# Optimization experiments

Measured on AMD Instinct MI355X. Metric: run time of the kernel, lower is better.

Reference implementation:

```python
import jax, jax.numpy as jnp
import numpy as np

N_NODES = 100000
N_EDGES = 3200000
F_IN = 128
F_OUT = 128


def setup_inputs() -> dict:
    key = jax.random.key(0)
    k1, k2, k3 = jax.random.split(key, 3)
    x = jax.random.normal(k1, (N_NODES, F_IN), dtype=jnp.float32)
    edge_index = jax.random.randint(k2, (2, N_EDGES), 0, N_NODES, dtype=jnp.int64)
    # xavier_uniform for weight, zeros for bias
    limit = float(np.sqrt(6.0 / (F_IN + F_OUT)))
    weight = jax.random.uniform(k3, (F_IN, F_OUT), dtype=jnp.float32,
                                minval=-limit, maxval=limit)
    bias = jnp.zeros((F_OUT,), dtype=jnp.float32)
    return {"x": x, "edge_index": edge_index, "weight": weight, "bias": bias}


def reference(x, edge_index, weight, bias):
    num_nodes = x.shape[0]
    # add self loops
    loops = jnp.arange(num_nodes, dtype=edge_index.dtype)
    row = jnp.concatenate([edge_index[0], loops])  # [E+N]
    col = jnp.concatenate([edge_index[1], loops])  # [E+N]
    # degree from row (matches torch.bincount(row))
    deg = jnp.zeros((num_nodes,), dtype=x.dtype).at[row].add(1.0)
    deg_inv_sqrt = jnp.where(deg > 0, jax.lax.rsqrt(jnp.maximum(deg, 1.0)), 0.0)
    norm = deg_inv_sqrt[row] * deg_inv_sqrt[col]  # [E+N]
    # dense transform then sparse aggregation (gather-scale-scatter)
    support = x @ weight  # [N, F_OUT]
    msgs = support[col] * norm[:, None]  # [E+N, F_OUT]
    out = jax.ops.segment_sum(msgs, row, num_segments=num_nodes)
    return out + bias
```

## Files before the change

kernel.cpp:

```cpp
#include <hip/hip_runtime.h>
#include <hip/hip_fp16.h>

#define FDIM 128
#define SCAN_B 1024
#define NCHK 128
#define NHALF 2
#define NFB (NHALF * NCHK)

typedef _Float16 half8 __attribute__((ext_vector_type(8)));
typedef float f32x4 __attribute__((ext_vector_type(4)));

__global__ void __launch_bounds__(1024) k_cnt(const int* __restrict__ row,
                                              unsigned char* __restrict__ cnt8,
                                              int nE, int n, int hspan) {
    __shared__ unsigned int h32[12544];
    int half  = blockIdx.x & (NHALF - 1);
    int chunk = blockIdx.x >> 1;
    int lo  = half * hspan;
    int len = min(hspan, n - lo);
    int nw  = (len + 3) >> 2;
    for (int j = threadIdx.x; j < nw; j += 1024) h32[j] = 0;
    __syncthreads();

    int per = (((nE + NCHK - 1) / NCHK) + 3) & ~3;
    int beg = chunk * per;
    int end = min(beg + per, nE);
    if (beg < end) {
        int nv = (end - beg) >> 2;
        const int4* row4 = reinterpret_cast<const int4*>(row + beg);
        for (int q = threadIdx.x; q < nv; q += 1024) {
            int4 r = row4[q];
            unsigned a;
            a = (unsigned)(r.x - lo); if (a < (unsigned)len) atomicAdd(&h32[a >> 2], 1u << ((a & 3) << 3));
            a = (unsigned)(r.y - lo); if (a < (unsigned)len) atomicAdd(&h32[a >> 2], 1u << ((a & 3) << 3));
            a = (unsigned)(r.z - lo); if (a < (unsigned)len) atomicAdd(&h32[a >> 2], 1u << ((a & 3) << 3));
            a = (unsigned)(r.w - lo); if (a < (unsigned)len) atomicAdd(&h32[a >> 2], 1u << ((a & 3) << 3));
        }
        for (int e = beg + (nv << 2) + threadIdx.x; e < end; e += 1024) {
            unsigned a = (unsigned)(row[e] - lo);
            if (a < (unsigned)len) atomicAdd(&h32[a >> 2], 1u << ((a & 3) << 3));
        }
    }
    __syncthreads();
    unsigned int* dst = reinterpret_cast<unsigned int*>(cnt8 + (size_t)chunk * n + lo);
    for (int j = threadIdx.x; j < nw; j += 1024) dst[j] = h32[j];
}

__global__ void __launch_bounds__(1024) k_scan_reduce(const unsigned char* __restrict__ cnt8,
                                                      int* __restrict__ part, int n) {
    __shared__ int sd[1024];
    int i = blockIdx.x * SCAN_B + threadIdx.x;
    int v = 0;
    if (i < n) {
        v = 1;
        const unsigned char* p = cnt8 + i;
        #pragma unroll 16
        for (int c = 0; c < NCHK; ++c) v += p[(size_t)c * n];
    }
    sd[threadIdx.x] = v;
    __syncthreads();
    for (int off = 512; off > 0; off >>= 1) {
        if (threadIdx.x < off) sd[threadIdx.x] += sd[threadIdx.x + off];
        __syncthreads();
    }
    if (threadIdx.x == 0) part[blockIdx.x] = sd[0];
}

__global__ void __launch_bounds__(1024) k_scan_final(unsigned char* __restrict__ cnt8,
                                                     const int* __restrict__ part,
                                                     int* __restrict__ offs,
                                                     float* __restrict__ dis,
                                                     int* __restrict__ sc,
                                                     int n, int nb) {
    __shared__ int sd[1024];
    __shared__ int sdp[128];
    int pv = 0;
    if (threadIdx.x < 128) {
        pv = (threadIdx.x < nb) ? part[threadIdx.x] : 0;
        sdp[threadIdx.x] = pv;
    }
    __syncthreads();
    for (int off = 1; off < 128; off <<= 1) {
        int t = 0;
        if (threadIdx.x < 128 && threadIdx.x >= off) t = sdp[threadIdx.x - off];
        __syncthreads();
        if (threadIdx.x < 128) sdp[threadIdx.x] += t;
        __syncthreads();
    }
    int blockbase = (blockIdx.x == 0) ? 0 : sdp[blockIdx.x - 1];

    int i = blockIdx.x * SCAN_B + threadIdx.x;
    int v = 0;
    if (i < n) {
        v = 1;
        const unsigned char* p = cnt8 + i;
        #pragma unroll 16
        for (int c = 0; c < NCHK; ++c) v += p[(size_t)c * n];
    }
    sd[threadIdx.x] = v;
    __syncthreads();
    for (int off = 1; off < 1024; off <<= 1) {
        int t = (threadIdx.x >= off) ? sd[threadIdx.x - off] : 0;
        __syncthreads();
        sd[threadIdx.x] += t;
        __syncthreads();
    }
    if (i < n) {
        int o = blockbase + sd[threadIdx.x] - v;
        offs[i] = o;
        if (i == n - 1) offs[n] = o + v;
        dis[i]  = rsqrtf((float)v);
        sc[o]   = i;
        unsigned char* p = cnt8 + i;
        int b = 1;
        #pragma unroll 16
        for (int c = 0; c < NCHK; ++c) {
            unsigned char cb = p[(size_t)c * n];
            p[(size_t)c * n] = (unsigned char)b;
            b += cb;
        }
    }
}

__global__ void __launch_bounds__(1024) k_fuse(const int* __restrict__ row,
                                               const int* __restrict__ col,
                                               unsigned char* __restrict__ cnt8,
                                               const int* __restrict__ offs,
                                               int* __restrict__ sc,
                                               const float* __restrict__ x,
                                               const float* __restrict__ w,
                                               const float* __restrict__ dis,
                                               __half* __restrict__ support,
                                               int nE, int n, int hspan) {
    __shared__ char smraw[65536];

    if (blockIdx.x < NFB) {
        unsigned int* cur32 = reinterpret_cast<unsigned int*>(smraw);
        int half  = blockIdx.x & (NHALF - 1);
        int chunk = blockIdx.x >> 1;
        int lo  = half * hspan;
        int len = min(hspan, n - lo);
        int nw  = (len + 3) >> 2;
        const unsigned int* src = reinterpret_cast<const unsigned int*>(
            cnt8 + (size_t)chunk * n + lo);
        for (int j = threadIdx.x; j < nw; j += 1024) cur32[j] = src[j];
        __syncthreads();

        int per = (((nE + NCHK - 1) / NCHK) + 3) & ~3;
        int beg = chunk * per;
        int end = min(beg + per, nE);
        if (beg < end) {
            int nv = (end - beg) >> 2;
            const int4* row4 = reinterpret_cast<const int4*>(row + beg);
            const int4* col4 = reinterpret_cast<const int4*>(col + beg);
            for (int q = threadIdx.x; q < nv; q += 1024) {
                int4 r  = row4[q];
                int4 cc = col4[q];
                unsigned a, old, sh;
                a = (unsigned)(r.x - lo);
                if (a < (unsigned)len) {
                    sh = (a & 3) << 3;
                    old = atomicAdd(&cur32[a >> 2], 1u << sh);
                    sc[offs[r.x] + (int)((old >> sh) & 255u)] = cc.x;
                }
                a = (unsigned)(r.y - lo);
                if (a < (unsigned)len) {
                    sh = (a & 3) << 3;
                    old = atomicAdd(&cur32[a >> 2], 1u << sh);
                    sc[offs[r.y] + (int)((old >> sh) & 255u)] = cc.y;
                }
                a = (unsigned)(r.z - lo);
                if (a < (unsigned)len) {
                    sh = (a & 3) << 3;
                    old = atomicAdd(&cur32[a >> 2], 1u << sh);
                    sc[offs[r.z] + (int)((old >> sh) & 255u)] = cc.z;
                }
                a = (unsigned)(r.w - lo);
                if (a < (unsigned)len) {
                    sh = (a & 3) << 3;
                    old = atomicAdd(&cur32[a >> 2], 1u << sh);
                    sc[offs[r.w] + (int)((old >> sh) & 255u)] = cc.w;
                }
            }
            for (int e = beg + (nv << 2) + threadIdx.x; e < end; e += 1024) {
                int r = row[e];
                unsigned a = (unsigned)(r - lo);
                if (a < (unsigned)len) {
                    unsigned sh = (a & 3) << 3;
                    unsigned old = atomicAdd(&cur32[a >> 2], 1u << sh);
                    sc[offs[r] + (int)((old >> sh) & 255u)] = col[e];
                }
            }
        }
    } else {
        half8* smw = reinterpret_cast<half8*>(smraw);
        for (int e = threadIdx.x; e < 2048; e += 1024) {
            int fid = e >> 6, lane = e & 63;
            int nt = fid >> 2, ks = fid & 3;
            int f  = nt * 16 + (lane & 15);
            int k0 = ks * 32 + (lane >> 4) * 8;
            half8 hi, lo;
            #pragma unroll
            for (int j = 0; j < 8; ++j) {
                float v = w[(size_t)(k0 + j) * FDIM + f];
                _Float16 h = (_Float16)v;
                hi[j] = h;
                lo[j] = (_Float16)(v - (float)h);
            }
            smw[e]        = hi;
            smw[2048 + e] = lo;
        }
        __syncthreads();

        int wave = threadIdx.x >> 6;
        int lane = threadIdx.x & 63;
        int wbase = (blockIdx.x - NFB) * 256 + wave * 16;
        if (wbase >= n) return;
        int r  = lane & 15;
        int kg = lane >> 4;

        int noder = min(wbase + r, n - 1);
        const float* xp = x + (size_t)noder * FDIM + kg * 8;
        half8 ah[4], al[4];
        #pragma unroll
        for (int ks = 0; ks < 4; ++ks) {
            const float4* p = reinterpret_cast<const float4*>(xp + ks * 32);
            float4 f0 = p[0], f1 = p[1];
            float v[8] = {f0.x, f0.y, f0.z, f0.w, f1.x, f1.y, f1.z, f1.w};
            #pragma unroll
            for (int j = 0; j < 8; ++j) {
                _Float16 h = (_Float16)v[j];
                ah[ks][j] = h;
                al[ks][j] = (_Float16)(v[j] - (float)h);
            }
        }

        float d[4];
        #pragma unroll
        for (int i = 0; i < 4; ++i)
            d[i] = dis[min(wbase + kg * 4 + i, n - 1)];

        #pragma unroll
        for (int nt = 0; nt < 8; ++nt) {
            const half8* bp = smw + (size_t)(nt * 4) * 64 + lane;
            f32x4 acc = {0.f, 0.f, 0.f, 0.f};
            #pragma unroll
            for (int ks = 0; ks < 4; ++ks) {
                half8 bh = bp[ks * 64];
                half8 bl = bp[2048 + ks * 64];
                acc = __builtin_amdgcn_mfma_f32_16x16x32_f16(ah[ks], bh, acc, 0, 0, 0);
                acc = __builtin_amdgcn_mfma_f32_16x16x32_f16(al[ks], bh, acc, 0, 0, 0);
                acc = __builtin_amdgcn_mfma_f32_16x16x32_f16(ah[ks], bl, acc, 0, 0, 0);
            }
            #pragma unroll
            for (int i = 0; i < 4; ++i) {
                int node = wbase + kg * 4 + i;
                if (node < n)
                    support[(size_t)node * FDIM + nt * 16 + r] =
                        __float2half(d[i] * acc[i]);
            }
        }
    }
}

__global__ void __launch_bounds__(64) k_agg(const __half2* __restrict__ sup2,
                                            const int* __restrict__ offs,
                                            const int* __restrict__ sc,
                                            const float* __restrict__ dis,
                                            const float* __restrict__ bias,
                                            float* __restrict__ out, int n) {
    int i  = blockIdx.x;
    int f2 = threadIdx.x;
    int beg = offs[i], end = offs[i + 1];
    float ax = 0.f, ay = 0.f;
    int j = beg;
    for (; j + 8 <= end; j += 8) {
        int c0 = sc[j],     c1 = sc[j + 1], c2 = sc[j + 2], c3 = sc[j + 3];
        int c4 = sc[j + 4], c5 = sc[j + 5], c6 = sc[j + 6], c7 = sc[j + 7];
        float2 v0 = __half22float2(sup2[(size_t)c0 * 64 + f2]);
        float2 v1 = __half22float2(sup2[(size_t)c1 * 64 + f2]);
        float2 v2 = __half22float2(sup2[(size_t)c2 * 64 + f2]);
        float2 v3 = __half22float2(sup2[(size_t)c3 * 64 + f2]);
        float2 v4 = __half22float2(sup2[(size_t)c4 * 64 + f2]);
        float2 v5 = __half22float2(sup2[(size_t)c5 * 64 + f2]);
        float2 v6 = __half22float2(sup2[(size_t)c6 * 64 + f2]);
        float2 v7 = __half22float2(sup2[(size_t)c7 * 64 + f2]);
        ax += ((v0.x + v1.x) + (v2.x + v3.x)) + ((v4.x + v5.x) + (v6.x + v7.x));
        ay += ((v0.y + v1.y) + (v2.y + v3.y)) + ((v4.y + v5.y) + (v6.y + v7.y));
    }
    for (; j + 4 <= end; j += 4) {
        int c0 = sc[j], c1 = sc[j + 1], c2 = sc[j + 2], c3 = sc[j + 3];
        float2 v0 = __half22float2(sup2[(size_t)c0 * 64 + f2]);
        float2 v1 = __half22float2(sup2[(size_t)c1 * 64 + f2]);
        float2 v2 = __half22float2(sup2[(size_t)c2 * 64 + f2]);
        float2 v3 = __half22float2(sup2[(size_t)c3 * 64 + f2]);
        ax += (v0.x + v1.x) + (v2.x + v3.x);
        ay += (v0.y + v1.y) + (v2.y + v3.y);
    }
    for (; j < end; ++j) {
        float2 v = __half22float2(sup2[(size_t)sc[j] * 64 + f2]);
        ax += v.x; ay += v.y;
    }
    float di = dis[i];
    const float2* b2 = reinterpret_cast<const float2*>(bias);
    float2 bb = b2[f2];
    float2 o;
    o.x = di * ax + bb.x;
    o.y = di * ay + bb.y;
    reinterpret_cast<float2*>(out)[(size_t)i * 64 + f2] = o;
}

extern "C" void kernel_launch(void* const* d_in, const int* in_sizes, int n_in,
                              void* d_out, int out_size, void* d_ws, size_t ws_size,
                              hipStream_t stream) {
    const float* x    = (const float*)d_in[0];
    const int*   ei   = (const int*)d_in[1];
    const float* w    = (const float*)d_in[2];
    const float* bias = (const float*)d_in[3];
    float*       out  = (float*)d_out;

    int n  = in_sizes[0] / FDIM;
    int nE = in_sizes[1] / 2;
    const int* row = ei;
    const int* col = ei + nE;
    int nbscan = (n + SCAN_B - 1) / SCAN_B;
    int hspan  = (((n + NHALF - 1) / NHALF) + 3) & ~3;
    int ngb    = (n + 255) / 256;

    char* ws = (char*)d_ws;
    size_t off = 0;
    auto alloc = [&](size_t bytes) -> void* {
        void* p = ws + off;
        off += (bytes + 255) & ~(size_t)255;
        return p;
    };
    __half*        support = (__half*)alloc((size_t)n * FDIM * sizeof(__half));
    unsigned char* cnt8    = (unsigned char*)alloc((size_t)NCHK * n + 16);
    int*           offs    = (int*)alloc((size_t)(n + 1) * sizeof(int));
    int*           part    = (int*)alloc((size_t)128 * sizeof(int));
    float*         dis     = (float*)alloc((size_t)n * sizeof(float));
    int*           sc      = (int*)alloc((size_t)(nE + n) * sizeof(int));

    k_cnt        <<<NFB, 1024, 0, stream>>>(row, cnt8, nE, n, hspan);
    k_scan_reduce<<<nbscan, 1024, 0, stream>>>(cnt8, part, n);
    k_scan_final <<<nbscan, 1024, 0, stream>>>(cnt8, part, offs, dis, sc, n, nbscan);
    k_fuse       <<<NFB + ngb, 1024, 0, stream>>>(row, col, cnt8, offs, sc,
                                                  x, w, dis, support, nE, n, hspan);
    k_agg        <<<n, 64, 0, stream>>>((const __half2*)support, offs,
                                        sc, dis, bias, out, n);
}
```

Measured before the change: 322.2 us.

## Split aggregation into two feature-half passes with wave-split edge lists

Aggregation now runs as two launches, each covering 64 of the 128 features. Within a wave, the two 32-lane halves each process alternate edges and are combined with a cross-lane shuffle. Each launch gathers a smaller working set (half of every support row), which is meant to improve cache hit rates for the random gathers. The cost is an extra launch, reading the index list twice, and 128-byte row segments per edge instead of 256-byte ones.

```diff
diff --git a/kernel.cpp b/kernel.cpp
--- a/kernel.cpp
+++ b/kernel.cpp
@@ -263,51 +263,44 @@
     }
 }
 
-__global__ void __launch_bounds__(64) k_agg(const __half2* __restrict__ sup2,
-                                            const int* __restrict__ offs,
-                                            const int* __restrict__ sc,
-                                            const float* __restrict__ dis,
-                                            const float* __restrict__ bias,
-                                            float* __restrict__ out, int n) {
-    int i  = blockIdx.x;
-    int f2 = threadIdx.x;
+__global__ void __launch_bounds__(64) k_aggh(const __half2* __restrict__ sup2,
+                                             const int* __restrict__ offs,
+                                             const int* __restrict__ sc,
+                                             const float* __restrict__ dis,
+                                             const float* __restrict__ bias,
+                                             float* __restrict__ out,
+                                             int n, int fb) {
+    int i    = blockIdx.x;
+    int lane = threadIdx.x;
+    int half = lane >> 5;
+    int l    = lane & 31;
     int beg = offs[i], end = offs[i + 1];
+    const __half2* sp = sup2 + fb + l;
     float ax = 0.f, ay = 0.f;
-    int j = beg;
-    for (; j + 8 <= end; j += 8) {
-        int c0 = sc[j],     c1 = sc[j + 1], c2 = sc[j + 2], c3 = sc[j + 3];
-        int c4 = sc[j + 4], c5 = sc[j + 5], c6 = sc[j + 6], c7 = sc[j + 7];
-        float2 v0 = __half22float2(sup2[(size_t)c0 * 64 + f2]);
-        float2 v1 = __half22float2(sup2[(size_t)c1 * 64 + f2]);
-        float2 v2 = __half22float2(sup2[(size_t)c2 * 64 + f2]);
-        float2 v3 = __half22float2(sup2[(size_t)c3 * 64 + f2]);
-        float2 v4 = __half22float2(sup2[(size_t)c4 * 64 + f2]);
-        float2 v5 = __half22float2(sup2[(size_t)c5 * 64 + f2]);
-        float2 v6 = __half22float2(sup2[(size_t)c6 * 64 + f2]);
-        float2 v7 = __half22float2(sup2[(size_t)c7 * 64 + f2]);
-        ax += ((v0.x + v1.x) + (v2.x + v3.x)) + ((v4.x + v5.x) + (v6.x + v7.x));
-        ay += ((v0.y + v1.y) + (v2.y + v3.y)) + ((v4.y + v5.y) + (v6.y + v7.y));
-    }
-    for (; j + 4 <= end; j += 4) {
-        int c0 = sc[j], c1 = sc[j + 1], c2 = sc[j + 2], c3 = sc[j + 3];
-        float2 v0 = __half22float2(sup2[(size_t)c0 * 64 + f2]);
-        float2 v1 = __half22float2(sup2[(size_t)c1 * 64 + f2]);
-        float2 v2 = __half22float2(sup2[(size_t)c2 * 64 + f2]);
-        float2 v3 = __half22float2(sup2[(size_t)c3 * 64 + f2]);
+    int j = beg + half;
+    for (; j + 6 < end; j += 8) {
+        int c0 = sc[j], c1 = sc[j + 2], c2 = sc[j + 4], c3 = sc[j + 6];
+        float2 v0 = __half22float2(sp[(size_t)c0 * 64]);
+        float2 v1 = __half22float2(sp[(size_t)c1 * 64]);
+        float2 v2 = __half22float2(sp[(size_t)c2 * 64]);
+        float2 v3 = __half22float2(sp[(size_t)c3 * 64]);
         ax += (v0.x + v1.x) + (v2.x + v3.x);
         ay += (v0.y + v1.y) + (v2.y + v3.y);
     }
-    for (; j < end; ++j) {
-        float2 v = __half22float2(sup2[(size_t)sc[j] * 64 + f2]);
+    for (; j < end; j += 2) {
+        float2 v = __half22float2(sp[(size_t)sc[j] * 64]);
         ax += v.x; ay += v.y;
     }
-    float di = dis[i];
-    const float2* b2 = reinterpret_cast<const float2*>(bias);
-    float2 bb = b2[f2];
-    float2 o;
-    o.x = di * ax + bb.x;
-    o.y = di * ay + bb.y;
-    reinterpret_cast<float2*>(out)[(size_t)i * 64 + f2] = o;
+    ax += __shfl_xor(ax, 32);
+    ay += __shfl_xor(ay, 32);
+    if (lane < 32) {
+        float di = dis[i];
+        float2 bb = reinterpret_cast<const float2*>(bias)[fb + l];
+        float2 o;
+        o.x = di * ax + bb.x;
+        o.y = di * ay + bb.y;
+        reinterpret_cast<float2*>(out)[(size_t)i * 64 + fb + l] = o;
+    }
 }
 
 extern "C" void kernel_launch(void* const* d_in, const int* in_sizes, int n_in,
@@ -346,6 +339,8 @@
     k_scan_final <<<nbscan, 1024, 0, stream>>>(cnt8, part, offs, dis, sc, n, nbscan);
     k_fuse       <<<NFB + ngb, 1024, 0, stream>>>(row, col, cnt8, offs, sc,
                                                   x, w, dis, support, nE, n, hspan);
-    k_agg        <<<n, 64, 0, stream>>>((const __half2*)support, offs,
-                                        sc, dis, bias, out, n);
-}
+    k_aggh       <<<n, 64, 0, stream>>>((const __half2*)support, offs,
+                                        sc, dis, bias, out, n, 0);
+    k_aggh       <<<n, 64, 0, stream>>>((const __half2*)support, offs,
+                                        sc, dis, bias, out, n, 32);
+}
```

Result: slower. 372.8 us (+15.7%).
